# Optimization experiments

Hardware: AMD Instinct MI355X
Metric: run time of the kernel (lower is better)

## Reference

```python
import jax, jax.numpy as jnp
import numpy as np

N_NODES = 100000
N_EDGES = 1600000
N_GRAPHS = 1024


def gcn_conv(x, W, b, src, dst, n_nodes):
    """PyG-style GCNConv: add self-loops, symmetric deg^-1/2 normalization,
    linear transform, scatter-add aggregation, bias."""
    h = x @ W  # [N, out]
    ones = jnp.ones(src.shape[0], dtype=h.dtype)
    deg = jax.ops.segment_sum(ones, dst, num_segments=n_nodes) + 1.0  # +1 self-loop
    dinv = jax.lax.rsqrt(deg)  # deg^-1/2, deg >= 1 so safe
    norm = dinv[src] * dinv[dst]  # [E]
    msg = h[src] * norm[:, None]  # gather + scale
    agg = jax.ops.segment_sum(msg, dst, num_segments=n_nodes)  # scatter-add
    # self-loop contribution: norm_ii = dinv_i^2
    return agg + h * (dinv * dinv)[:, None] + b


def setup_inputs() -> dict:
    key = jax.random.key(0)
    ks = jax.random.split(key, 12)
    x = jax.random.normal(ks[0], (N_NODES, 5), dtype=jnp.float32)
    src = jax.random.randint(ks[1], (N_EDGES,), 0, N_NODES)
    dst = jax.random.randint(ks[2], (N_EDGES,), 0, N_NODES)
    batch = jnp.sort(jax.random.randint(ks[3], (N_NODES,), 0, N_GRAPHS))
    def glorot(k, shp):
        lim = float(np.sqrt(6.0 / (shp[0] + shp[1])))
        return jax.random.uniform(k, shp, jnp.float32, -lim, lim)
    return {
        "x": x, "src": src, "dst": dst, "batch": batch,
        "W1": glorot(ks[4], (5, 16)),  "b1": jnp.zeros((16,), jnp.float32),
        "W2": glorot(ks[5], (16, 32)), "b2": jnp.zeros((32,), jnp.float32),
        "W3": glorot(ks[6], (32, 64)), "b3": jnp.zeros((64,), jnp.float32),
        "Wfc": glorot(ks[7], (64, 2)), "bfc": jnp.zeros((2,), jnp.float32),
    }


def reference(x, src, dst, batch, W1, b1, W2, b2, W3, b3, Wfc, bfc):
    h = jax.nn.relu(gcn_conv(x, W1, b1, src, dst, N_NODES))
    h = jax.nn.relu(gcn_conv(h, W2, b2, src, dst, N_NODES))
    h = jax.nn.relu(gcn_conv(h, W3, b3, src, dst, N_NODES))
    # global mean pool over graphs
    summed = jax.ops.segment_sum(h, batch, num_segments=N_GRAPHS)  # [G, 64]
    counts = jax.ops.segment_sum(jnp.ones(h.shape[0], h.dtype), batch, num_segments=N_GRAPHS)
    pooled = summed / jnp.maximum(counts, 1.0)[:, None]
    logits = pooled @ Wfc + bfc  # [G, 2]
    return jax.nn.log_softmax(logits, axis=1)
```

## Files before the change

### kernel.cpp

```cpp
#include <hip/hip_runtime.h>


#define BLK 256
#define CH 4096
#define EPT (CH / BLK)
#define NB 256
#define GSH 9
#define GSZ 512


__device__ inline float bfu_lo(unsigned int w) { return __uint_as_float(w << 16); }
__device__ inline float bfu_hi(unsigned int w) { return __uint_as_float(w & 0xffff0000u); }
__device__ inline unsigned int f2bf(float f) {
    unsigned int w = __float_as_uint(f);
    return (w + 0x7fffu + ((w >> 16) & 1u)) >> 16;
}
__device__ inline unsigned int pack2(float a, float b) {
    return f2bf(a) | (f2bf(b) << 16);
}


__global__ void hist1_kernel(const int* __restrict__ dst, int* __restrict__ cnt,
                             int E, int nChunks) {
    __shared__ int h[NB];
    int t = threadIdx.x, b = blockIdx.x;
    h[t] = 0;
    __syncthreads();
    int base = b * CH;
#pragma unroll
    for (int j = 0; j < EPT; ++j) {
        int e = base + j * BLK + t;
        if (e < E) atomicAdd(&h[dst[e] >> GSH], 1);
    }
    __syncthreads();
    cnt[(size_t)t * nChunks + b] = h[t];
}

__global__ void seg_scan_kernel(int* __restrict__ cnt, int* __restrict__ bucketTot,
                                int nChunks) {
    __shared__ int part[256];
    int b = blockIdx.x, t = threadIdx.x;
    size_t base = (size_t)b * nChunks;
    int per = (nChunks + 255) / 256;
    int lo = t * per, hi = lo + per < nChunks ? lo + per : nChunks;
    int sum = 0;
    for (int i = lo; i < hi; ++i) sum += cnt[base + i];
    part[t] = sum;
    __syncthreads();
    for (int off = 1; off < 256; off <<= 1) {
        int x = (t >= off) ? part[t - off] : 0;
        __syncthreads();
        if (t >= off) part[t] += x;
        __syncthreads();
    }
    int run = part[t] - sum;
    for (int i = lo; i < hi; ++i) { int v = cnt[base + i]; cnt[base + i] = run; run += v; }
    if (t == 255) bucketTot[b] = part[255];
}

__global__ void bucket_scan_kernel(const int* __restrict__ bucketTot,
                                   int* __restrict__ groupBeg, int E) {
    __shared__ int part[256];
    int t = threadIdx.x;
    int v = bucketTot[t];
    part[t] = v;
    __syncthreads();
    for (int off = 1; off < 256; off <<= 1) {
        int x = (t >= off) ? part[t - off] : 0;
        __syncthreads();
        if (t >= off) part[t] += x;
        __syncthreads();
    }
    groupBeg[t] = part[t] - v;
    if (t == 0) groupBeg[NB] = E;
}

__global__ void scatter1_kernel(const int* __restrict__ src, const int* __restrict__ dst,
                                const int* __restrict__ cnt, const int* __restrict__ groupBeg,
                                int* __restrict__ pe, int E, int nChunks) {
    __shared__ int offs[NB];
    int t = threadIdx.x, b = blockIdx.x;
    offs[t] = cnt[(size_t)t * nChunks + b] + groupBeg[t];
    __syncthreads();
    int base = b * CH;
#pragma unroll
    for (int j = 0; j < EPT; ++j) {
        int e = base + j * BLK + t;
        if (e < E) {
            int d = dst[e];
            int p = atomicAdd(&offs[d >> GSH], 1);
            pe[p] = ((d & (GSZ - 1)) << 17) | src[e];
        }
    }
}


__global__ void group_csr_kernel(const int* __restrict__ pe, const int* __restrict__ groupBeg,
                                 int* __restrict__ col, int* __restrict__ row_ptr,
                                 float* __restrict__ dinv, const float* __restrict__ x,
                                 uint4* __restrict__ xa, int N, int E) {
    __shared__ int hist[GSZ];
    __shared__ int scn[GSZ];
    __shared__ int part[256];
    int g = blockIdx.x, t = threadIdx.x;
    hist[t] = 0; hist[t + 256] = 0;
    __syncthreads();
    int lo = groupBeg[g], hi = groupBeg[g + 1];
    for (int e = lo + t; e < hi; e += BLK)
        atomicAdd(&hist[pe[e] >> 17], 1);
    __syncthreads();
    int a0 = hist[2 * t], a1 = hist[2 * t + 1];
    int s2 = a0 + a1;
    part[t] = s2;
    __syncthreads();
    for (int off = 1; off < 256; off <<= 1) {
        int xx = (t >= off) ? part[t - off] : 0;
        __syncthreads();
        if (t >= off) part[t] += xx;
        __syncthreads();
    }
    int excl = part[t] - s2;
    scn[2 * t] = excl;
    scn[2 * t + 1] = excl + a0;
    __syncthreads();
#pragma unroll
    for (int i = t; i < GSZ; i += BLK) {
        int d = (g << GSH) + i;
        if (d < N) {
            row_ptr[d] = lo + scn[i];
            float di = rsqrtf((float)hist[i] + 1.0f);
            dinv[d] = di;
            const float* r = x + (size_t)d * 5;
            uint4 u;
            u.x = pack2(r[0] * di, r[1] * di);
            u.y = pack2(r[2] * di, r[3] * di);
            u.z = pack2(r[4] * di, 0.f);
            u.w = 0u;
            xa[d] = u;
        }
    }
    if (g == 0 && t == 0) row_ptr[N] = E;
    __syncthreads();
    hist[t] = scn[t]; hist[t + 256] = scn[t + 256];
    __syncthreads();
    for (int e = lo + t; e < hi; e += BLK) {
        int v = pe[e];
        int p = atomicAdd(&hist[v >> 17], 1);
        col[lo + p] = v & 0x1FFFF;
    }
}


template <int F, int FIN, int FOUT, int CAP, bool PRESCALE_OUT>
__global__ void fused_layer_kernel(const int* __restrict__ row_ptr, const int* __restrict__ col,
                                   const uint4* __restrict__ xb, const float* __restrict__ W,
                                   const float* __restrict__ bias, const float* __restrict__ dinv,
                                   uint2* __restrict__ outb, int N) {
    constexpr int TPN = F / 8;
    constexpr int NPB = 256 / TPN;
    constexpr int RQ  = F / 8;
    constexpr int QO  = FOUT / 4;
    constexpr int STR = F + 1;
    __shared__ int lcol[CAP];
    __shared__ int lrp[NPB + 1];
    __shared__ float dl[NPB];
    __shared__ __align__(16) float gl[NPB * STR];
    __shared__ __align__(16) float wl[FIN * FOUT];
    __shared__ __align__(16) float bl[FOUT];
    int t = threadIdx.x;
    int n0 = blockIdx.x * NPB;
    for (int i = t; i <= NPB; i += 256) lrp[i] = row_ptr[min(n0 + i, N)];
    for (int i = t; i < NPB; i += 256) dl[i] = dinv[min(n0 + i, N - 1)];
    for (int i = t; i < FIN * FOUT / 4; i += 256)
        ((float4*)wl)[i] = ((const float4*)W)[i];
    for (int i = t; i < FOUT; i += 256) bl[i] = bias[i];
    __syncthreads();
    int base = lrp[0];
    int total = lrp[NPB] - base;
    int stage = total < CAP ? total : CAP;
    for (int i = t; i < stage; i += 256) lcol[i] = col[base + i];
    __syncthreads();
    {
        int ln = t / TPN, q = t % TPN;
        int n = n0 + ln;
        if (n < N) {
            float acc[8];
            uint4 u = xb[(size_t)n * RQ + q];
            acc[0] = bfu_lo(u.x); acc[1] = bfu_hi(u.x);
            acc[2] = bfu_lo(u.y); acc[3] = bfu_hi(u.y);
            acc[4] = bfu_lo(u.z); acc[5] = bfu_hi(u.z);
            acc[6] = bfu_lo(u.w); acc[7] = bfu_hi(u.w);
            int beg = lrp[ln] - base, end = lrp[ln + 1] - base;
            int stop = end < stage ? end : stage;
            int e = beg;
            for (; e + 7 < stop; e += 8) {
                uint4 uu[8];
#pragma unroll
                for (int j = 0; j < 8; ++j) uu[j] = xb[(size_t)lcol[e + j] * RQ + q];
#pragma unroll
                for (int j = 0; j < 8; ++j) {
                    acc[0] += bfu_lo(uu[j].x); acc[1] += bfu_hi(uu[j].x);
                    acc[2] += bfu_lo(uu[j].y); acc[3] += bfu_hi(uu[j].y);
                    acc[4] += bfu_lo(uu[j].z); acc[5] += bfu_hi(uu[j].z);
                    acc[6] += bfu_lo(uu[j].w); acc[7] += bfu_hi(uu[j].w);
                }
            }
            for (; e + 3 < stop; e += 4) {
                uint4 uu[4];
#pragma unroll
                for (int j = 0; j < 4; ++j) uu[j] = xb[(size_t)lcol[e + j] * RQ + q];
#pragma unroll
                for (int j = 0; j < 4; ++j) {
                    acc[0] += bfu_lo(uu[j].x); acc[1] += bfu_hi(uu[j].x);
                    acc[2] += bfu_lo(uu[j].y); acc[3] += bfu_hi(uu[j].y);
                    acc[4] += bfu_lo(uu[j].z); acc[5] += bfu_hi(uu[j].z);
                    acc[6] += bfu_lo(uu[j].w); acc[7] += bfu_hi(uu[j].w);
                }
            }
            for (; e < end; ++e) {
                int s = (e < stage) ? lcol[e] : col[base + e];
                uint4 uu = xb[(size_t)s * RQ + q];
                acc[0] += bfu_lo(uu.x); acc[1] += bfu_hi(uu.x);
                acc[2] += bfu_lo(uu.y); acc[3] += bfu_hi(uu.y);
                acc[4] += bfu_lo(uu.z); acc[5] += bfu_hi(uu.z);
                acc[6] += bfu_lo(uu.w); acc[7] += bfu_hi(uu.w);
            }
            float* gr = gl + ln * STR + q * 8;
#pragma unroll
            for (int j = 0; j < 8; ++j) gr[j] = acc[j];
        }
    }
    __syncthreads();
    for (int task = t; task < NPB * QO; task += 256) {
        int ln2 = task / QO, qq = task % QO;
        int n2 = n0 + ln2;
        if (n2 >= N) continue;
        float di = dl[ln2];
        const float* row = gl + ln2 * STR;
        float4 acc = make_float4(0.f, 0.f, 0.f, 0.f);
#pragma unroll
        for (int k = 0; k < FIN; ++k) {
            float rk = row[k];
            float4 wk = *(const float4*)(wl + k * FOUT + 4 * qq);
            acc.x = fmaf(rk, wk.x, acc.x);
            acc.y = fmaf(rk, wk.y, acc.y);
            acc.z = fmaf(rk, wk.z, acc.z);
            acc.w = fmaf(rk, wk.w, acc.w);
        }
        float4 bq = *(const float4*)(bl + 4 * qq);
        float4 v;
        v.x = fmaxf(di * acc.x + bq.x, 0.f);
        v.y = fmaxf(di * acc.y + bq.y, 0.f);
        v.z = fmaxf(di * acc.z + bq.z, 0.f);
        v.w = fmaxf(di * acc.w + bq.w, 0.f);
        if (PRESCALE_OUT) { v.x *= di; v.y *= di; v.z *= di; v.w *= di; }
        uint2 o;
        o.x = pack2(v.x, v.y);
        o.y = pack2(v.z, v.w);
        outb[(size_t)n2 * QO + qq] = o;
    }
}


__global__ void bounds_kernel(const int* __restrict__ batch, int* __restrict__ start,
                              int N, int G) {
    int g = blockIdx.x * blockDim.x + threadIdx.x;
    if (g > G) return;
    if (g == G) { start[G] = N; return; }
    int lo = 0, hi = N;
    while (lo < hi) {
        int mid = (lo + hi) >> 1;
        if (batch[mid] < g) lo = mid + 1; else hi = mid;
    }
    start[g] = lo;
}

__global__ void pool_head_kernel(const unsigned int* __restrict__ h, const int* __restrict__ start,
                                 const float* __restrict__ Wfc, const float* __restrict__ bfc,
                                 float* __restrict__ out) {
    __shared__ float part[8][64];
    int g = blockIdx.x;
    int t = threadIdx.x;
    int u = t & 31, w = t >> 5;
    int s = start[g], e = start[g + 1];
    float a0 = 0.f, a1 = 0.f;
    for (int n = s + w; n < e; n += 8) {
        unsigned int word = h[(size_t)n * 32 + u];
        a0 += bfu_lo(word);
        a1 += bfu_hi(word);
    }
    part[w][2 * u]     = a0;
    part[w][2 * u + 1] = a1;
    __syncthreads();
    if (t < 64) {
        float p = 0.f;
#pragma unroll
        for (int w2 = 0; w2 < 8; ++w2) p += part[w2][t];
        p /= fmaxf((float)(e - s), 1.0f);
        float l0 = p * Wfc[t * 2 + 0];
        float l1 = p * Wfc[t * 2 + 1];
#pragma unroll
        for (int off = 32; off; off >>= 1) {
            l0 += __shfl_down(l0, off);
            l1 += __shfl_down(l1, off);
        }
        if (t == 0) {
            l0 += bfc[0]; l1 += bfc[1];
            float m   = fmaxf(l0, l1);
            float lse = m + logf(expf(l0 - m) + expf(l1 - m));
            out[g * 2 + 0] = l0 - lse;
            out[g * 2 + 1] = l1 - lse;
        }
    }
}


extern "C" void kernel_launch(void* const* d_in, const int* in_sizes, int n_in,
                              void* d_out, int out_size, void* d_ws, size_t ws_size,
                              hipStream_t stream) {
    const float* x     = (const float*)d_in[0];
    const int*   src   = (const int*)d_in[1];
    const int*   dst   = (const int*)d_in[2];
    const int*   batch = (const int*)d_in[3];
    const float* W1    = (const float*)d_in[4];
    const float* b1    = (const float*)d_in[5];
    const float* W2    = (const float*)d_in[6];
    const float* b2    = (const float*)d_in[7];
    const float* W3    = (const float*)d_in[8];
    const float* b3    = (const float*)d_in[9];
    const float* Wfc   = (const float*)d_in[10];
    const float* bfc   = (const float*)d_in[11];
    float* out = (float*)d_out;

    const int N = in_sizes[0] / 5;
    const int E = in_sizes[1];
    const int G = out_size / 2;

    const int nChunks = (E + CH - 1) / CH;
    const int M       = NB * nChunks;
    const int Mpad    = (M + 3) & ~3;
    const int nGroups = (N + GSZ - 1) / GSZ;

    int* row_ptr  = (int*)d_ws;
    int* col      = row_ptr + N + 4;
    int* cnt      = col + E;
    int* groupBeg = cnt + Mpad;
    int* bucketTot= groupBeg + 260;
    int* start    = bucketTot + 256;
    float* dinv   = (float*)(start + G + 8);
    int*   Xa     = (int*)(dinv + N);
    int*   Xb     = Xa + (size_t)N * 16;
    int*   H3b    = Xb + (size_t)N * 8;
    int*   pe     = H3b;

    auto blocks = [](long n) { return (int)((n + BLK - 1) / BLK); };

    hist1_kernel<<<nChunks, 256, 0, stream>>>(dst, cnt, E, nChunks);
    seg_scan_kernel<<<NB, 256, 0, stream>>>(cnt, bucketTot, nChunks);
    bucket_scan_kernel<<<1, 256, 0, stream>>>(bucketTot, groupBeg, E);
    scatter1_kernel<<<nChunks, 256, 0, stream>>>(src, dst, cnt, groupBeg, pe, E, nChunks);
    group_csr_kernel<<<nGroups, 256, 0, stream>>>(pe, groupBeg, col, row_ptr, dinv,
                                                  x, (uint4*)Xa, N, E);

    bounds_kernel<<<blocks(G + 1), BLK, 0, stream>>>(batch, start, N, G);

    fused_layer_kernel<8, 5, 16, 5120, true><<<(N + 255) / 256, 256, 0, stream>>>(
        row_ptr, col, (const uint4*)Xa, W1, b1, dinv, (uint2*)Xb, N);

    fused_layer_kernel<16, 16, 32, 3072, true><<<(N + 127) / 128, 256, 0, stream>>>(
        row_ptr, col, (const uint4*)Xb, W2, b2, dinv, (uint2*)Xa, N);

    fused_layer_kernel<32, 32, 64, 1536, false><<<(N + 63) / 64, 256, 0, stream>>>(
        row_ptr, col, (const uint4*)Xa, W3, b3, dinv, (uint2*)H3b, N);

    pool_head_kernel<<<G, 256, 0, stream>>>((const unsigned int*)H3b, start, Wfc, bfc, out);
}
```

Before: 129.9 us.

## Fold bucket scan and graph bounds kernels into consumers, halve chunk size

Removes the single-block bucket_scan kernel by having each scatter and group_csr block redundantly recompute the 256-entry exclusive scan of bucket totals. It also removes bounds_kernel by having pool_head blocks binary-search their own graph start and end. The chunk size is halved, which doubles the number of scatter/hist blocks and the size of the count matrix. This saves two kernel launches but adds redundant scan work and more chunk bookkeeping.

Measured after the change: 130.8 us. About the same (+0.7%).

```diff
diff --git a/kernel.cpp b/kernel.cpp
--- a/kernel.cpp
+++ b/kernel.cpp
@@ -2,7 +2,7 @@
 
 
 #define BLK 256
-#define CH 4096
+#define CH 2048
 #define EPT (CH / BLK)
 #define NB 256
 #define GSH 9
@@ -58,12 +58,14 @@
     if (t == 255) bucketTot[b] = part[255];
 }
 
-__global__ void bucket_scan_kernel(const int* __restrict__ bucketTot,
-                                   int* __restrict__ groupBeg, int E) {
+__global__ void scatter1_kernel(const int* __restrict__ src, const int* __restrict__ dst,
+                                const int* __restrict__ cnt, const int* __restrict__ bucketTot,
+                                int* __restrict__ pe, int E, int nChunks) {
+    __shared__ int offs[NB];
     __shared__ int part[256];
-    int t = threadIdx.x;
-    int v = bucketTot[t];
-    part[t] = v;
+    int t = threadIdx.x, b = blockIdx.x;
+    int c = bucketTot[t];
+    part[t] = c;
     __syncthreads();
     for (int off = 1; off < 256; off <<= 1) {
         int x = (t >= off) ? part[t - off] : 0;
@@ -71,16 +73,7 @@
         if (t >= off) part[t] += x;
         __syncthreads();
     }
-    groupBeg[t] = part[t] - v;
-    if (t == 0) groupBeg[NB] = E;
-}
-
-__global__ void scatter1_kernel(const int* __restrict__ src, const int* __restrict__ dst,
-                                const int* __restrict__ cnt, const int* __restrict__ groupBeg,
-                                int* __restrict__ pe, int E, int nChunks) {
-    __shared__ int offs[NB];
-    int t = threadIdx.x, b = blockIdx.x;
-    offs[t] = cnt[(size_t)t * nChunks + b] + groupBeg[t];
+    offs[t] = cnt[(size_t)t * nChunks + b] + (part[t] - c);
     __syncthreads();
     int base = b * CH;
 #pragma unroll
@@ -95,17 +88,29 @@
 }
 
 
-__global__ void group_csr_kernel(const int* __restrict__ pe, const int* __restrict__ groupBeg,
+__global__ void group_csr_kernel(const int* __restrict__ pe, const int* __restrict__ bucketTot,
                                  int* __restrict__ col, int* __restrict__ row_ptr,
                                  float* __restrict__ dinv, const float* __restrict__ x,
                                  uint4* __restrict__ xa, int N, int E) {
     __shared__ int hist[GSZ];
     __shared__ int scn[GSZ];
     __shared__ int part[256];
+    __shared__ int sh_lo, sh_hi;
     int g = blockIdx.x, t = threadIdx.x;
+    int c = bucketTot[t];
+    part[t] = c;
+    __syncthreads();
+    for (int off = 1; off < 256; off <<= 1) {
+        int v = (t >= off) ? part[t - off] : 0;
+        __syncthreads();
+        if (t >= off) part[t] += v;
+        __syncthreads();
+    }
+    if (t == g) { sh_lo = part[t] - c; sh_hi = part[t]; }
+    __syncthreads();
+    int lo = sh_lo, hi = sh_hi;
     hist[t] = 0; hist[t + 256] = 0;
     __syncthreads();
-    int lo = groupBeg[g], hi = groupBeg[g + 1];
     for (int e = lo + t; e < hi; e += BLK)
         atomicAdd(&hist[pe[e] >> 17], 1);
     __syncthreads();
@@ -262,27 +267,26 @@
 }
 
 
-__global__ void bounds_kernel(const int* __restrict__ batch, int* __restrict__ start,
-                              int N, int G) {
-    int g = blockIdx.x * blockDim.x + threadIdx.x;
-    if (g > G) return;
-    if (g == G) { start[G] = N; return; }
-    int lo = 0, hi = N;
-    while (lo < hi) {
-        int mid = (lo + hi) >> 1;
-        if (batch[mid] < g) lo = mid + 1; else hi = mid;
-    }
-    start[g] = lo;
-}
-
-__global__ void pool_head_kernel(const unsigned int* __restrict__ h, const int* __restrict__ start,
+__global__ void pool_head_kernel(const unsigned int* __restrict__ h,
+                                 const int* __restrict__ batch,
                                  const float* __restrict__ Wfc, const float* __restrict__ bfc,
-                                 float* __restrict__ out) {
+                                 float* __restrict__ out, int N, int G) {
     __shared__ float part[8][64];
+    __shared__ int se[2];
     int g = blockIdx.x;
     int t = threadIdx.x;
+    if (t < 2) {
+        int target = g + t;
+        int lo = 0, hi = N;
+        while (lo < hi) {
+            int mid = (lo + hi) >> 1;
+            if (batch[mid] < target) lo = mid + 1; else hi = mid;
+        }
+        se[t] = lo;
+    }
+    __syncthreads();
+    int s = se[0], e = se[1];
     int u = t & 31, w = t >> 5;
-    int s = start[g], e = start[g + 1];
     float a0 = 0.f, a1 = 0.f;
     for (int n = s + w; n < e; n += 8) {
         unsigned int word = h[(size_t)n * 32 + u];
@@ -344,25 +348,18 @@
     int* row_ptr  = (int*)d_ws;
     int* col      = row_ptr + N + 4;
     int* cnt      = col + E;
-    int* groupBeg = cnt + Mpad;
-    int* bucketTot= groupBeg + 260;
-    int* start    = bucketTot + 256;
-    float* dinv   = (float*)(start + G + 8);
+    int* bucketTot= cnt + Mpad;
+    float* dinv   = (float*)(bucketTot + 256);
     int*   Xa     = (int*)(dinv + N);
     int*   Xb     = Xa + (size_t)N * 16;
     int*   H3b    = Xb + (size_t)N * 8;
     int*   pe     = H3b;
 
-    auto blocks = [](long n) { return (int)((n + BLK - 1) / BLK); };
-
     hist1_kernel<<<nChunks, 256, 0, stream>>>(dst, cnt, E, nChunks);
     seg_scan_kernel<<<NB, 256, 0, stream>>>(cnt, bucketTot, nChunks);
-    bucket_scan_kernel<<<1, 256, 0, stream>>>(bucketTot, groupBeg, E);
-    scatter1_kernel<<<nChunks, 256, 0, stream>>>(src, dst, cnt, groupBeg, pe, E, nChunks);
-    group_csr_kernel<<<nGroups, 256, 0, stream>>>(pe, groupBeg, col, row_ptr, dinv,
+    scatter1_kernel<<<nChunks, 256, 0, stream>>>(src, dst, cnt, bucketTot, pe, E, nChunks);
+    group_csr_kernel<<<nGroups, 256, 0, stream>>>(pe, bucketTot, col, row_ptr, dinv,
                                                   x, (uint4*)Xa, N, E);
-
-    bounds_kernel<<<blocks(G + 1), BLK, 0, stream>>>(batch, start, N, G);
 
     fused_layer_kernel<8, 5, 16, 5120, true><<<(N + 255) / 256, 256, 0, stream>>>(
         row_ptr, col, (const uint4*)Xa, W1, b1, dinv, (uint2*)Xb, N);
@@ -373,5 +370,6 @@
     fused_layer_kernel<32, 32, 64, 1536, false><<<(N + 63) / 64, 256, 0, stream>>>(
         row_ptr, col, (const uint4*)Xa, W3, b3, dinv, (uint2*)H3b, N);
 
-    pool_head_kernel<<<G, 256, 0, stream>>>((const unsigned int*)H3b, start, Wfc, bfc, out);
-}
+    pool_head_kernel<<<G, 256, 0, stream>>>((const unsigned int*)H3b, batch,
+                                            Wfc, bfc, out, N, G);
+}
```
